# Kernel tuning notes

Hardware: AMD Instinct MI355X
Metric: run time of the kernel (lower is better)

The kernel has to match this reference:

```python
import jax, jax.numpy as jnp
import numpy as np

N = 100000
E = 1600000
IN_C = 128
HID = 64
OUT_C = 112


def setup_inputs() -> dict:
    key = jax.random.key(0)
    ks = jax.random.split(key, 10)
    x = jax.random.normal(ks[0], (N, IN_C), dtype=jnp.float32)
    edge_index = jax.random.randint(ks[1], (2, E), 0, N, dtype=jnp.int32)
    s1 = 1.0 / np.sqrt(IN_C)
    s2 = 1.0 / np.sqrt(HID)
    return {
        "x": x,
        "edge_index": edge_index,
        "W1l": jax.random.uniform(ks[2], (IN_C, HID), jnp.float32, -s1, s1),
        "b1": jnp.zeros((HID,), jnp.float32),
        "W1r": jax.random.uniform(ks[3], (IN_C, HID), jnp.float32, -s1, s1),
        "W2l": jax.random.uniform(ks[4], (HID, HID), jnp.float32, -s2, s2),
        "b2": jnp.zeros((HID,), jnp.float32),
        "W2r": jax.random.uniform(ks[5], (HID, HID), jnp.float32, -s2, s2),
        "Wo": jax.random.uniform(ks[6], (HID, OUT_C), jnp.float32, -s2, s2),
        "bo": jnp.zeros((OUT_C,), jnp.float32),
    }


def _sage_conv(x, src, dst, Wl, b, Wr):
    # mean-aggregate neighbor messages (src -> dst), then linear + root linear
    msg = x[src]                                             # [E, F] gather
    agg = jax.ops.segment_sum(msg, dst, num_segments=N)      # [N, F] scatter-add
    deg = jax.ops.segment_sum(jnp.ones((src.shape[0],), x.dtype), dst, num_segments=N)
    mean = agg / jnp.maximum(deg, 1.0)[:, None]
    return mean @ Wl + b + x @ Wr


def reference(x, edge_index, W1l, b1, W1r, W2l, b2, W2r, Wo, bo):
    src, dst = edge_index[0], edge_index[1]
    h = jax.nn.relu(_sage_conv(x, src, dst, W1l, b1, W1r))
    # dropout disabled (inference / eval mode)
    h = jax.nn.relu(_sage_conv(h, src, dst, W2l, b2, W2r))
    return h @ Wo + bo
```

## Files before the change

### kernel.cpp

```cpp
#include <hip/hip_runtime.h>

typedef float f32x4 __attribute__((ext_vector_type(4)));
typedef short s16x8 __attribute__((ext_vector_type(8)));
typedef short s16x4 __attribute__((ext_vector_type(4)));

#define BSTRIDE 9216

__device__ __forceinline__ unsigned short f2bf(float f) {
    unsigned u = __builtin_bit_cast(unsigned, f);
    unsigned r = (u + 0x7FFFu + ((u >> 16) & 1u)) >> 16;
    return (unsigned short)r;
}
__device__ __forceinline__ float bf2f(unsigned short h) {
    unsigned u = ((unsigned)h) << 16;
    return __builtin_bit_cast(float, u);
}
__device__ __forceinline__ float bflo(unsigned u) {
    return __builtin_bit_cast(float, u << 16);
}
__device__ __forceinline__ float bfhi(unsigned u) {
    return __builtin_bit_cast(float, u & 0xffff0000u);
}

__global__ __launch_bounds__(256)
void pack_frags(const float* __restrict__ W1l, const float* __restrict__ W1r,
                const float* __restrict__ W2l, const float* __restrict__ W2r,
                const float* __restrict__ Wo,
                short* __restrict__ PH1, short* __restrict__ PL1,
                short* __restrict__ PH2, short* __restrict__ PL2,
                short* __restrict__ PHo, short* __restrict__ PLo,
                int* __restrict__ gcursor, int nbkt)
{
    if (blockIdx.x == 0)
        for (int i = threadIdx.x; i < nbkt; i += 256) gcursor[i] = 0;
    const int tot = 2048 + 1024 + 896;
    for (int e = blockIdx.x * 256 + threadIdx.x; e < tot; e += gridDim.x * 256) {
        int lane, f, k0, c, stride;
        const float* W;
        short *PH, *PL;
        int idx;
        if (e < 2048) {
            idx = e; lane = e & 63; f = e >> 6;
            int kt = f & 3, ct = (f >> 2) & 3, m = f >> 4;
            W = m ? W1r : W1l; PH = PH1; PL = PL1;
            k0 = kt * 32 + ((lane >> 4) << 3);
            c  = ct * 16 + (lane & 15);
            stride = 64;
        } else if (e < 3072) {
            int e2 = e - 2048;
            idx = e2; lane = e2 & 63; f = e2 >> 6;
            int kt = f & 1, ct = (f >> 1) & 3, m = f >> 3;
            W = m ? W2r : W2l; PH = PH2; PL = PL2;
            k0 = kt * 32 + ((lane >> 4) << 3);
            c  = ct * 16 + (lane & 15);
            stride = 64;
        } else {
            int eo = e - 3072;
            idx = eo; lane = eo & 63; f = eo >> 6;
            int kt = f & 1, ct = f >> 1;
            W = Wo; PH = PHo; PL = PLo;
            k0 = kt * 32 + ((lane >> 4) << 3);
            c  = ct * 16 + (lane & 15);
            stride = 112;
        }
        short h[8], l[8];
        #pragma unroll
        for (int j = 0; j < 8; ++j) {
            float v = W[(size_t)(k0 + j) * stride + c];
            unsigned short hb = f2bf(v);
            h[j] = (short)hb;
            l[j] = (short)f2bf(v - bf2f(hb));
        }
        #pragma unroll
        for (int j = 0; j < 8; ++j) { PH[idx * 8 + j] = h[j]; PL[idx * 8 + j] = l[j]; }
    }
}

__global__ __launch_bounds__(512)
void fused_gemm1_scatter(const float* __restrict__ X, const short* __restrict__ PH,
                         const short* __restrict__ PL, unsigned short* __restrict__ Yl,
                         unsigned short* __restrict__ Yr, int n,
                         const int* __restrict__ src, const int* __restrict__ dst,
                         int* __restrict__ gcursor, int* __restrict__ packed,
                         int E, int B, int sctBlocks)
{
    __shared__ unsigned short sT[8][16 * 72];
    __shared__ int lh[256];
    __shared__ int lbase[256];

    if ((int)blockIdx.x < sctBlocks) {
        for (int i = threadIdx.x; i < B; i += 512) lh[i] = 0;
        __syncthreads();
        long base = (long)blockIdx.x * 8192;
        int bkt[16], rnk[16], pk[16];
        #pragma unroll
        for (int j = 0; j < 16; ++j) {
            long e = base + j * 512 + threadIdx.x;
            if (e < E) {
                int d = dst[e], s = src[e];
                bkt[j] = d >> 9;
                pk[j]  = (s << 9) | (d & 511);
                rnk[j] = atomicAdd(&lh[bkt[j]], 1);
            } else bkt[j] = -1;
        }
        __syncthreads();
        for (int i = threadIdx.x; i < B; i += 512) {
            int v = lh[i];
            lbase[i] = v ? atomicAdd(&gcursor[i], v) : 0;
        }
        __syncthreads();
        #pragma unroll
        for (int j = 0; j < 16; ++j)
            if (bkt[j] >= 0)
                packed[(size_t)bkt[j] * BSTRIDE + lbase[bkt[j]] + rnk[j]] = pk[j];
        return;
    }

    constexpr int K = 128, NKT = 4;
    const int lane = threadIdx.x & 63;
    const int wid  = threadIdx.x >> 6;
    const long ntile = ((long)n + 15) >> 4;
    long t = (long)(blockIdx.x - sctBlocks) * 8 + wid;
    if (t >= ntile) return;
    const long rbase = t << 4;
    long arow = rbase + (lane & 15);
    if (arow >= n) arow = n - 1;
    const int koff = (lane >> 4) << 3;
    const float* xr = X + arow * K + koff;

    s16x8 Bh[NKT], Bl[NKT];
    #pragma unroll
    for (int kt = 0; kt < NKT; ++kt) {
        f32x4 a0 = *(const f32x4*)(xr + kt * 32);
        f32x4 a1 = *(const f32x4*)(xr + kt * 32 + 4);
        s16x8 h, l;
        #pragma unroll
        for (int j = 0; j < 4; ++j) {
            float v = a0[j]; unsigned short hb = f2bf(v);
            h[j] = (short)hb; l[j] = (short)f2bf(v - bf2f(hb));
            float v2 = a1[j]; unsigned short hb2 = f2bf(v2);
            h[4 + j] = (short)hb2; l[4 + j] = (short)f2bf(v2 - bf2f(hb2));
        }
        Bh[kt] = h; Bl[kt] = l;
    }

    f32x4 acc[2][4];
    #pragma unroll
    for (int m = 0; m < 2; ++m)
        #pragma unroll
        for (int ct = 0; ct < 4; ++ct) acc[m][ct] = (f32x4)(0.f);

    #pragma unroll
    for (int m = 0; m < 2; ++m)
    #pragma unroll
    for (int ct = 0; ct < 4; ++ct)
    #pragma unroll
    for (int kt = 0; kt < NKT; ++kt) {
        const int fidx = ((((m << 2) | ct) * NKT) + kt) * 64 + lane;
        s16x8 Ah = *(const s16x8*)(PH + (size_t)fidx * 8);
        s16x8 Al = *(const s16x8*)(PL + (size_t)fidx * 8);
        acc[m][ct] = __builtin_amdgcn_mfma_f32_16x16x32_bf16(Ah, Bh[kt], acc[m][ct], 0, 0, 0);
        acc[m][ct] = __builtin_amdgcn_mfma_f32_16x16x32_bf16(Al, Bh[kt], acc[m][ct], 0, 0, 0);
        acc[m][ct] = __builtin_amdgcn_mfma_f32_16x16x32_bf16(Ah, Bl[kt], acc[m][ct], 0, 0, 0);
    }

    const int wrow = lane & 15, q4 = (lane >> 4) << 2;
    #pragma unroll
    for (int m = 0; m < 2; ++m) {
        unsigned short* __restrict__ Y = m ? Yr : Yl;
        #pragma unroll
        for (int ct = 0; ct < 4; ++ct) {
            s16x4 pv;
            #pragma unroll
            for (int j = 0; j < 4; ++j) pv[j] = (short)f2bf(acc[m][ct][j]);
            *(s16x4*)&sT[wid][wrow * 72 + ct * 16 + q4] = pv;
        }
        asm volatile("s_waitcnt lgkmcnt(0)" ::: "memory");
        if (rbase + 16 <= (long)n) {
            #pragma unroll
            for (int s = 0; s < 2; ++s) {
                int f = s * 64 + lane;
                s16x8 v = *(const s16x8*)&sT[wid][(f >> 3) * 72 + ((f & 7) << 3)];
                *(s16x8*)&Y[rbase * 64 + (size_t)f * 8] = v;
            }
        } else {
            #pragma unroll
            for (int s = 0; s < 2; ++s) {
                int f = s * 64 + lane;
                s16x8 v = *(const s16x8*)&sT[wid][(f >> 3) * 72 + ((f & 7) << 3)];
                long g = rbase * 64 + (size_t)f * 8;
                #pragma unroll
                for (int jj = 0; jj < 8; ++jj)
                    if (g + jj < (long)n * 64) Y[g + jj] = (unsigned short)v[jj];
            }
        }
        asm volatile("s_waitcnt lgkmcnt(0)" ::: "memory");
    }
}

__global__ __launch_bounds__(256)
void hist_scan(const int* __restrict__ packed, const int* __restrict__ cnts,
               int* __restrict__ degi, int* __restrict__ rowptrP,
               int* __restrict__ partial, int n)
{
    __shared__ int h[512];
    __shared__ int s[256];
    const int b = blockIdx.x, t = threadIdx.x, nb = b << 9;
    int cnt = n - nb; if (cnt > 512) cnt = 512;
    for (int i = t; i < 512; i += 256) h[i] = 0;
    __syncthreads();
    int bs = b * BSTRIDE, be = bs + cnts[b];
    for (int i = bs + t; i < be; i += 256)
        atomicAdd(&h[packed[i] & 511], 1);
    __syncthreads();
    int e0 = (2 * t     < cnt) ? h[2 * t]     : 0;
    int e1 = (2 * t + 1 < cnt) ? h[2 * t + 1] : 0;
    int p0 = (e0 + 7) & ~7;
    int p1 = (e1 + 7) & ~7;
    int mysum = p0 + p1;
    s[t] = mysum;
    __syncthreads();
    for (int off = 1; off < 256; off <<= 1) {
        int u = (t >= off) ? s[t - off] : 0;
        __syncthreads();
        s[t] += u;
        __syncthreads();
    }
    int excl = s[t] - mysum;
    if (2 * t < cnt)     { degi[nb + 2 * t]     = e0; rowptrP[nb + 2 * t]     = excl; }
    if (2 * t + 1 < cnt) { degi[nb + 2 * t + 1] = e1; rowptrP[nb + 2 * t + 1] = excl + p0; }
    if (t == 255) partial[b] = s[255];
}

__global__ void scan_partials(int* __restrict__ partial, int B)
{
    __shared__ int s[256];
    int t = threadIdx.x;
    int v = (t < B) ? partial[t] : 0;
    s[t] = v;
    __syncthreads();
    for (int off = 1; off < 256; off <<= 1) {
        int u = (t >= off) ? s[t - off] : 0;
        __syncthreads();
        s[t] += u;
        __syncthreads();
    }
    if (t < B) partial[t] = s[t] - v;
    if (t == 255) partial[B] = s[255];
}

__global__ __launch_bounds__(256)
void bucket_fill_final(const int* __restrict__ packed, const int* __restrict__ cnts,
                       const int* __restrict__ partial, int* __restrict__ rowptrP,
                       int* __restrict__ csr, unsigned* __restrict__ Adummy,
                       int n, int nbkt, int dummyOff)
{
    __shared__ int cur[512];
    __shared__ int rs[513];
    const int b = blockIdx.x, t = threadIdx.x, nb = b << 9;
    int cnt = n - nb; if (cnt > 512) cnt = 512;
    const int base = partial[b];
    for (int i = t; i < cnt; i += 256) {
        int v = rowptrP[nb + i] + base;
        rowptrP[nb + i] = v;
        cur[i] = v;
        rs[i] = v;
    }
    if (t == 0) rs[cnt] = partial[b + 1];
    if (b == 0) {
        if (t == 0) rowptrP[n] = partial[nbkt];
        if (t < 32) Adummy[t] = 0u;
    }
    __syncthreads();
    int bs = b * BSTRIDE, be = bs + cnts[b];
    for (int i = bs + t; i < be; i += 256) {
        int p = packed[i];
        int pos = atomicAdd(&cur[p & 511], 1);
        csr[pos] = (p >> 9) << 7;
    }
    __syncthreads();
    for (int i = t; i < cnt; i += 256) {
        int end = rs[i + 1];
        for (int p = cur[i]; p < end; ++p) csr[p] = dummyOff;
    }
}

__global__ __launch_bounds__(256)
void pull_agg_pad(const unsigned short* __restrict__ feat, const int* __restrict__ rowptrP,
                  const int* __restrict__ degi, const int* __restrict__ csrB,
                  const unsigned short* __restrict__ C, const float* __restrict__ bias,
                  unsigned short* __restrict__ H, int n)
{
    const int lane = threadIdx.x & 63;
    const int half = lane >> 5;
    const int c    = lane & 31;
    const int wid  = threadIdx.x >> 6;
    const char* fb = (const char*)feat;
    const int cb   = c << 2;
    const float2 bv = *(const float2*)&bias[c * 2];

    const long w  = (long)blockIdx.x * 4 + wid;
    const long nw = (long)gridDim.x * 4;
    for (long rp = w * 2; rp < n; rp += nw * 2) {
        int2 rr = *(const int2*)&rowptrP[rp];
        int eB = (rp + 1 < n) ? rowptrP[rp + 2] : rr.y;

        const long r = rp + half;
        int dg = 1; unsigned cu = 0;
        if (r < n) {
            dg = degi[r];
            cu = *(const unsigned*)&C[(size_t)r * 64 + (c << 1)];
        }

        int iA = rr.x + (half << 2);
        int iB = rr.y + (half << 2);
        const int endA = rr.y, endB = eB;
        bool dA = iA < endA, dB = iB < endB;
        int4 oA = (int4)(0), oB = (int4)(0);
        if (dA) oA = *(const int4*)&csrB[iA];
        if (dB) oB = *(const int4*)&csrB[iB];

        float a0A = 0.f, a1A = 0.f, a0B = 0.f, a1B = 0.f;
        while (dA | dB) {
            unsigned uA0, uA1, uA2, uA3, uB0, uB1, uB2, uB3;
            if (dA) {
                uA0 = *(const unsigned*)(fb + oA.x + cb);
                uA1 = *(const unsigned*)(fb + oA.y + cb);
                uA2 = *(const unsigned*)(fb + oA.z + cb);
                uA3 = *(const unsigned*)(fb + oA.w + cb);
            }
            if (dB) {
                uB0 = *(const unsigned*)(fb + oB.x + cb);
                uB1 = *(const unsigned*)(fb + oB.y + cb);
                uB2 = *(const unsigned*)(fb + oB.z + cb);
                uB3 = *(const unsigned*)(fb + oB.w + cb);
            }
            int niA = iA + 8, niB = iB + 8;
            bool ndA = niA < endA, ndB = niB < endB;
            int4 tA = oA, tB = oB;
            if (ndA) tA = *(const int4*)&csrB[niA];
            if (ndB) tB = *(const int4*)&csrB[niB];
            if (dA) {
                a0A += bflo(uA0); a1A += bfhi(uA0);
                a0A += bflo(uA1); a1A += bfhi(uA1);
                a0A += bflo(uA2); a1A += bfhi(uA2);
                a0A += bflo(uA3); a1A += bfhi(uA3);
            }
            if (dB) {
                a0B += bflo(uB0); a1B += bfhi(uB0);
                a0B += bflo(uB1); a1B += bfhi(uB1);
                a0B += bflo(uB2); a1B += bfhi(uB2);
                a0B += bflo(uB3); a1B += bfhi(uB3);
            }
            oA = tA; oB = tB; iA = niA; iB = niB; dA = ndA; dB = ndB;
        }

        a0A += __shfl_xor(a0A, 32, 64);
        a1A += __shfl_xor(a1A, 32, 64);
        a0B += __shfl_xor(a0B, 32, 64);
        a1B += __shfl_xor(a1B, 32, 64);

        if (r < n) {
            float m0 = half ? a0B : a0A;
            float m1 = half ? a1B : a1A;
            float d = (float)dg;
            d = d > 1.f ? d : 1.f;
            float inv = 1.f / d;
            float v0 = m0 * inv + bflo(cu) + bv.x;
            float v1 = m1 * inv + bfhi(cu) + bv.y;
            v0 = v0 > 0.f ? v0 : 0.f;
            v1 = v1 > 0.f ? v1 : 0.f;
            unsigned pv = (unsigned)f2bf(v0) | ((unsigned)f2bf(v1) << 16);
            *(unsigned*)&H[(size_t)r * 64 + (c << 1)] = pv;
        }
    }
}


__global__ __launch_bounds__(512)
void dual_gemm_b16in(const unsigned short* __restrict__ X, const short* __restrict__ PH,
                     const short* __restrict__ PL, unsigned short* __restrict__ Yl,
                     unsigned short* __restrict__ Yr, int n)
{
    constexpr int NKT = 2;
    __shared__ unsigned short sT[8][16 * 72];
    const int lane = threadIdx.x & 63;
    const int wid  = threadIdx.x >> 6;
    const long ntile = ((long)n + 15) >> 4;
    long t = (long)blockIdx.x * 8 + wid;
    if (t >= ntile) return;
    const long rbase = t << 4;
    long arow = rbase + (lane & 15);
    if (arow >= n) arow = n - 1;
    const int koff = (lane >> 4) << 3;
    const unsigned short* xr = X + arow * 64 + koff;

    s16x8 Bv[NKT];
    #pragma unroll
    for (int kt = 0; kt < NKT; ++kt) Bv[kt] = *(const s16x8*)(xr + kt * 32);

    f32x4 acc[2][4];
    #pragma unroll
    for (int m = 0; m < 2; ++m)
        #pragma unroll
        for (int ct = 0; ct < 4; ++ct) acc[m][ct] = (f32x4)(0.f);

    #pragma unroll
    for (int m = 0; m < 2; ++m)
    #pragma unroll
    for (int ct = 0; ct < 4; ++ct)
    #pragma unroll
    for (int kt = 0; kt < NKT; ++kt) {
        const int fidx = ((((m << 2) | ct) * NKT) + kt) * 64 + lane;
        s16x8 Ah = *(const s16x8*)(PH + (size_t)fidx * 8);
        s16x8 Al = *(const s16x8*)(PL + (size_t)fidx * 8);
        acc[m][ct] = __builtin_amdgcn_mfma_f32_16x16x32_bf16(Ah, Bv[kt], acc[m][ct], 0, 0, 0);
        acc[m][ct] = __builtin_amdgcn_mfma_f32_16x16x32_bf16(Al, Bv[kt], acc[m][ct], 0, 0, 0);
    }

    const int wrow = lane & 15, q4 = (lane >> 4) << 2;
    #pragma unroll
    for (int m = 0; m < 2; ++m) {
        unsigned short* __restrict__ Y = m ? Yr : Yl;
        #pragma unroll
        for (int ct = 0; ct < 4; ++ct) {
            s16x4 pv;
            #pragma unroll
            for (int j = 0; j < 4; ++j) pv[j] = (short)f2bf(acc[m][ct][j]);
            *(s16x4*)&sT[wid][wrow * 72 + ct * 16 + q4] = pv;
        }
        asm volatile("s_waitcnt lgkmcnt(0)" ::: "memory");
        if (rbase + 16 <= (long)n) {
            #pragma unroll
            for (int s = 0; s < 2; ++s) {
                int f = s * 64 + lane;
                s16x8 v = *(const s16x8*)&sT[wid][(f >> 3) * 72 + ((f & 7) << 3)];
                *(s16x8*)&Y[rbase * 64 + (size_t)f * 8] = v;
            }
        } else {
            #pragma unroll
            for (int s = 0; s < 2; ++s) {
                int f = s * 64 + lane;
                s16x8 v = *(const s16x8*)&sT[wid][(f >> 3) * 72 + ((f & 7) << 3)];
                long g = rbase * 64 + (size_t)f * 8;
                #pragma unroll
                for (int jj = 0; jj < 8; ++jj)
                    if (g + jj < (long)n * 64) Y[g + jj] = (unsigned short)v[jj];
            }
        }
        asm volatile("s_waitcnt lgkmcnt(0)" ::: "memory");
    }
}

__global__ __launch_bounds__(512)
void gemm_out_mfma(const unsigned short* __restrict__ X, const short* __restrict__ PH,
                   const short* __restrict__ PL, const float* __restrict__ bo,
                   float* __restrict__ Y, int n)
{
    constexpr int NCT = 7;
    __shared__ float sT[8][16 * 120];
    const int lane = threadIdx.x & 63;
    const int wid  = threadIdx.x >> 6;
    const long ntile = ((long)n + 15) >> 4;
    long t = (long)blockIdx.x * 8 + wid;
    if (t >= ntile) return;
    const long rbase = t << 4;
    long arow = rbase + (lane & 15);
    if (arow >= n) arow = n - 1;
    const int koff = (lane >> 4) << 3;
    const unsigned short* xr = X + arow * 64 + koff;

    s16x8 Bv[2];
    #pragma unroll
    for (int kt = 0; kt < 2; ++kt) Bv[kt] = *(const s16x8*)(xr + kt * 32);

    f32x4 acc[NCT];
    #pragma unroll
    for (int ct = 0; ct < NCT; ++ct) acc[ct] = (f32x4)(0.f);

    #pragma unroll
    for (int ct = 0; ct < NCT; ++ct)
    #pragma unroll
    for (int kt = 0; kt < 2; ++kt) {
        const int fidx = (ct * 2 + kt) * 64 + lane;
        s16x8 Ah = *(const s16x8*)(PH + (size_t)fidx * 8);
        s16x8 Al = *(const s16x8*)(PL + (size_t)fidx * 8);
        acc[ct] = __builtin_amdgcn_mfma_f32_16x16x32_bf16(Ah, Bv[kt], acc[ct], 0, 0, 0);
        acc[ct] = __builtin_amdgcn_mfma_f32_16x16x32_bf16(Al, Bv[kt], acc[ct], 0, 0, 0);
    }

    const int wrow = lane & 15, q4 = (lane >> 4) << 2;
    #pragma unroll
    for (int ct = 0; ct < NCT; ++ct)
        *(f32x4*)&sT[wid][wrow * 120 + ct * 16 + q4] = acc[ct];
    asm volatile("s_waitcnt lgkmcnt(0)" ::: "memory");

    if (rbase + 16 <= (long)n) {
        #pragma unroll
        for (int s = 0; s < 7; ++s) {
            int f = s * 64 + lane;
            int row = f / 28, ch = f % 28;
            f32x4 v = *(const f32x4*)&sT[wid][row * 120 + ch * 4];
            f32x4 b4 = *(const f32x4*)&bo[ch * 4];
            v.x += b4.x; v.y += b4.y; v.z += b4.z; v.w += b4.w;
            *(f32x4*)&Y[rbase * 112 + (size_t)f * 4] = v;
        }
    } else {
        #pragma unroll
        for (int s = 0; s < 7; ++s) {
            int f = s * 64 + lane;
            int row = f / 28, ch = f % 28;
            f32x4 v = *(const f32x4*)&sT[wid][row * 120 + ch * 4];
            #pragma unroll
            for (int jj = 0; jj < 4; ++jj) {
                long g = rbase * 112 + (size_t)f * 4 + jj;
                if (g < (long)n * 112) Y[g] = v[jj] + bo[ch * 4 + jj];
            }
        }
    }
}


extern "C" void kernel_launch(void* const* d_in, const int* in_sizes, int n_in,
                              void* d_out, int out_size, void* d_ws, size_t ws_size,
                              hipStream_t stream)
{
    const float* x   = (const float*)d_in[0];
    const int*   ei  = (const int*)d_in[1];
    const float* W1l = (const float*)d_in[2];
    const float* b1  = (const float*)d_in[3];
    const float* W1r = (const float*)d_in[4];
    const float* W2l = (const float*)d_in[5];
    const float* b2  = (const float*)d_in[6];
    const float* W2r = (const float*)d_in[7];
    const float* Wo  = (const float*)d_in[8];
    const float* bo  = (const float*)d_in[9];
    float* out = (float*)d_out;

    const int n = in_sizes[0] / 128;
    const int E = in_sizes[1] / 2;
    const int* srcI = ei;
    const int* dstI = ei + E;
    const int nbkt   = (n + 511) >> 9;
    const size_t nn64 = (size_t)n * 64;
    const size_t csrCap = (size_t)E + (size_t)8 * n + 16;

    unsigned short* A = (unsigned short*)d_ws;
    unsigned short* C = A + nn64 + 64;
    unsigned short* H = C + nn64;
    int*   rowptrP= (int*)(H + nn64);
    int*   degi   = rowptrP + n + 1;
    int*   partial= degi + n;
    int*   csr    = partial + 260;
    int*   packed = csr + csrCap;
    int*   gcursor= packed + (size_t)nbkt * BSTRIDE;
    short* PH1    = (short*)(gcursor + nbkt);
    short* PL1    = PH1 + 16384;
    short* PH2    = PL1 + 16384;
    short* PL2    = PH2 + 8192;
    short* PHo    = PL2 + 8192;
    short* PLo    = PHo + 7168;

    const long ntile = ((long)n + 15) >> 4;
    const int gmf = (int)((ntile + 7) / 8);
    const int sctBlocks = (int)((E + 8191) / 8192);

    pack_frags<<<16, 256, 0, stream>>>(W1l, W1r, W2l, W2r, Wo,
                                       PH1, PL1, PH2, PL2, PHo, PLo, gcursor, nbkt);

    fused_gemm1_scatter<<<sctBlocks + gmf, 512, 0, stream>>>(
        x, PH1, PL1, A, C, n, srcI, dstI, gcursor, packed, E, nbkt, sctBlocks);

    hist_scan<<<nbkt, 256, 0, stream>>>(packed, gcursor, degi, rowptrP, partial, n);
    scan_partials<<<1, 256, 0, stream>>>(partial, nbkt);
    bucket_fill_final<<<nbkt, 256, 0, stream>>>(packed, gcursor, partial, rowptrP,
                                                csr, (unsigned*)(A + nn64), n, nbkt, n << 7);

    pull_agg_pad<<<4096, 256, 0, stream>>>(A, rowptrP, degi, csr, C, b1, H, n);

    dual_gemm_b16in<<<gmf, 512, 0, stream>>>(H, PH2, PL2, A, C, n);
    pull_agg_pad<<<4096, 256, 0, stream>>>(A, rowptrP, degi, csr, C, b2, H, n);

    gemm_out_mfma<<<gmf, 512, 0, stream>>>(H, PHo, PLo, bo, out, n);
}
```

Before: 180.7 us.

## Fold partial scan into bucket fill, reorder fused blocks, shrink scatter chunks

Drops the single-block scan_partials launch. Each bucket_fill_final block now computes its own exclusive prefix by reducing the preceding partials in shared memory, which removes one kernel launch and its dependency bubble. The fused GEMM/scatter kernel now places GEMM blocks first and scatter blocks after, and each scatter block handles 2048 edges instead of 8192. That gives more, smaller scatter blocks for better balance across CUs, at the cost of more global atomics on the bucket cursors.

```diff
diff --git a/kernel.cpp b/kernel.cpp
--- a/kernel.cpp
+++ b/kernel.cpp
@@ -82,19 +82,19 @@
                          unsigned short* __restrict__ Yr, int n,
                          const int* __restrict__ src, const int* __restrict__ dst,
                          int* __restrict__ gcursor, int* __restrict__ packed,
-                         int E, int B, int sctBlocks)
+                         int E, int B, int gemmBlocks)
 {
     __shared__ unsigned short sT[8][16 * 72];
     __shared__ int lh[256];
     __shared__ int lbase[256];
 
-    if ((int)blockIdx.x < sctBlocks) {
+    if ((int)blockIdx.x >= gemmBlocks) {
         for (int i = threadIdx.x; i < B; i += 512) lh[i] = 0;
         __syncthreads();
-        long base = (long)blockIdx.x * 8192;
-        int bkt[16], rnk[16], pk[16];
-        #pragma unroll
-        for (int j = 0; j < 16; ++j) {
+        long base = (long)(blockIdx.x - gemmBlocks) * 2048;
+        int bkt[4], rnk[4], pk[4];
+        #pragma unroll
+        for (int j = 0; j < 4; ++j) {
             long e = base + j * 512 + threadIdx.x;
             if (e < E) {
                 int d = dst[e], s = src[e];
@@ -110,7 +110,7 @@
         }
         __syncthreads();
         #pragma unroll
-        for (int j = 0; j < 16; ++j)
+        for (int j = 0; j < 4; ++j)
             if (bkt[j] >= 0)
                 packed[(size_t)bkt[j] * BSTRIDE + lbase[bkt[j]] + rnk[j]] = pk[j];
         return;
@@ -120,7 +120,7 @@
     const int lane = threadIdx.x & 63;
     const int wid  = threadIdx.x >> 6;
     const long ntile = ((long)n + 15) >> 4;
-    long t = (long)(blockIdx.x - sctBlocks) * 8 + wid;
+    long t = (long)blockIdx.x * 8 + wid;
     if (t >= ntile) return;
     const long rbase = t << 4;
     long arow = rbase + (lane & 15);
@@ -232,23 +232,6 @@
     if (t == 255) partial[b] = s[255];
 }
 
-__global__ void scan_partials(int* __restrict__ partial, int B)
-{
-    __shared__ int s[256];
-    int t = threadIdx.x;
-    int v = (t < B) ? partial[t] : 0;
-    s[t] = v;
-    __syncthreads();
-    for (int off = 1; off < 256; off <<= 1) {
-        int u = (t >= off) ? s[t - off] : 0;
-        __syncthreads();
-        s[t] += u;
-        __syncthreads();
-    }
-    if (t < B) partial[t] = s[t] - v;
-    if (t == 255) partial[B] = s[255];
-}
-
 __global__ __launch_bounds__(256)
 void bucket_fill_final(const int* __restrict__ packed, const int* __restrict__ cnts,
                        const int* __restrict__ partial, int* __restrict__ rowptrP,
@@ -257,21 +240,32 @@
 {
     __shared__ int cur[512];
     __shared__ int rs[513];
+    __shared__ int red[256];
     const int b = blockIdx.x, t = threadIdx.x, nb = b << 9;
     int cnt = n - nb; if (cnt > 512) cnt = 512;
-    const int base = partial[b];
+
+    int loc = 0;
+    for (int j = t; j < b; j += 256) loc += partial[j];
+    red[t] = loc;
+    __syncthreads();
+    for (int off = 128; off > 0; off >>= 1) {
+        if (t < off) red[t] += red[t + off];
+        __syncthreads();
+    }
+    const int base = red[0];
+    const int bend = base + partial[b];
+
     for (int i = t; i < cnt; i += 256) {
         int v = rowptrP[nb + i] + base;
         rowptrP[nb + i] = v;
         cur[i] = v;
         rs[i] = v;
     }
-    if (t == 0) rs[cnt] = partial[b + 1];
-    if (b == 0) {
-        if (t == 0) rowptrP[n] = partial[nbkt];
-        if (t < 32) Adummy[t] = 0u;
-    }
+    if (t == 0) rs[cnt] = bend;
+    if (b == nbkt - 1 && t == 0) rowptrP[n] = bend;
+    if (b == 0 && t < 32) Adummy[t] = 0u;
     __syncthreads();
+
     int bs = b * BSTRIDE, be = bs + cnts[b];
     for (int i = bs + t; i < be; i += 256) {
         int p = packed[i];
@@ -563,16 +557,15 @@
 
     const long ntile = ((long)n + 15) >> 4;
     const int gmf = (int)((ntile + 7) / 8);
-    const int sctBlocks = (int)((E + 8191) / 8192);
+    const int sctBlocks = (int)((E + 2047) / 2048);
 
     pack_frags<<<16, 256, 0, stream>>>(W1l, W1r, W2l, W2r, Wo,
                                        PH1, PL1, PH2, PL2, PHo, PLo, gcursor, nbkt);
 
-    fused_gemm1_scatter<<<sctBlocks + gmf, 512, 0, stream>>>(
-        x, PH1, PL1, A, C, n, srcI, dstI, gcursor, packed, E, nbkt, sctBlocks);
+    fused_gemm1_scatter<<<gmf + sctBlocks, 512, 0, stream>>>(
+        x, PH1, PL1, A, C, n, srcI, dstI, gcursor, packed, E, nbkt, gmf);
 
     hist_scan<<<nbkt, 256, 0, stream>>>(packed, gcursor, degi, rowptrP, partial, n);
-    scan_partials<<<1, 256, 0, stream>>>(partial, nbkt);
     bucket_fill_final<<<nbkt, 256, 0, stream>>>(packed, gcursor, partial, rowptrP,
                                                 csr, (unsigned*)(A + nn64), n, nbkt, n << 7);
 
```

After: 188.8 us. +4.5%, slower.
